# Kernel tuning notes

Hardware: AMD Instinct MI355X
Metric: run time of the kernel (lower is better)

Reference implementation:

```python
import jax, jax.numpy as jnp
import numpy as np

N_NODES = 20000
N_EDGES = 320000
D_IN = 256      # n_source_nodes (input feature dim)
HEADS = 4
HEAD_DIM = 64   # n_target_nodes // heads
D_OUT = HEADS * HEAD_DIM  # n_target_nodes = 256
EDGE_DIM = 1


def setup_inputs() -> dict:
    key = jax.random.key(0)
    ks = jax.random.split(key, 12)
    s = 0.05
    return {
        "x": jax.random.normal(ks[0], (N_NODES, D_IN), jnp.float32),
        "edge_index": jax.random.randint(ks[1], (2, N_EDGES), 0, N_NODES, jnp.int64),
        "edge_attr": jax.random.normal(ks[2], (N_EDGES, EDGE_DIM), jnp.float32),
        # TransformerConv params (weights stored [in, out]; PyG Linear defaults: q/k/v have bias, edge lin has no bias, skip lin has bias)
        "Wq": jax.random.normal(ks[3], (D_IN, D_OUT), jnp.float32) * s,
        "bq": jnp.zeros((D_OUT,), jnp.float32),
        "Wk": jax.random.normal(ks[4], (D_IN, D_OUT), jnp.float32) * s,
        "bk": jnp.zeros((D_OUT,), jnp.float32),
        "Wv": jax.random.normal(ks[5], (D_IN, D_OUT), jnp.float32) * s,
        "bv": jnp.zeros((D_OUT,), jnp.float32),
        "We": jax.random.normal(ks[6], (EDGE_DIM, D_OUT), jnp.float32) * s,
        "Wskip": jax.random.normal(ks[7], (D_IN, D_OUT), jnp.float32) * s,
        "bskip": jnp.zeros((D_OUT,), jnp.float32),
        # GraphNorm params
        "gn_weight": jnp.ones((D_OUT,), jnp.float32),
        "gn_bias": jnp.zeros((D_OUT,), jnp.float32),
        "gn_mean_scale": jnp.ones((D_OUT,), jnp.float32),
    }


def reference(x, edge_index, edge_attr, Wq, bq, Wk, bk, Wv, bv, We, Wskip, bskip, gn_weight, gn_bias, gn_mean_scale):
    N = x.shape[0]
    src, dst = edge_index[0], edge_index[1]  # message flows src -> dst (source_to_target)

    q = (x @ Wq + bq).reshape(N, HEADS, HEAD_DIM)
    k = (x @ Wk + bk).reshape(N, HEADS, HEAD_DIM)
    v = (x @ Wv + bv).reshape(N, HEADS, HEAD_DIM)
    e = (edge_attr @ We).reshape(-1, HEADS, HEAD_DIM)  # [E, H, C]

    k_j = k[src] + e                                   # [E, H, C]
    alpha = jnp.einsum('ehc,ehc->eh', q[dst], k_j) / jnp.sqrt(jnp.float32(HEAD_DIM))

    # segment softmax over edges sharing the same target node
    a_max = jax.ops.segment_max(alpha, dst, num_segments=N)[dst]
    a_exp = jnp.exp(alpha - a_max)
    a_sum = jax.ops.segment_sum(a_exp, dst, num_segments=N)[dst]
    att = a_exp / (a_sum + 1e-16)                      # [E, H]

    msg = (v[src] + e) * att[..., None]                # [E, H, C]
    out = jax.ops.segment_sum(msg, dst, num_segments=N).reshape(N, D_OUT)
    out = out + x @ Wskip + bskip                      # root/skip connection (beta=False)

    # GraphNorm (single graph): weight*(x - alpha*mean)/sqrt(var+eps) + bias
    mean = out.mean(axis=0)
    centered = out - gn_mean_scale * mean
    var = jnp.mean(centered * centered, axis=0)
    out = gn_weight * centered * jax.lax.rsqrt(var + 1e-5) + gn_bias

    out = jax.nn.relu(out)
    xt = out.T @ out                                   # [D_OUT, D_OUT]
    xt_min, xt_max = jnp.min(xt), jnp.max(xt)
    return (xt - xt_min) / (xt_max - xt_min + 1e-8)
```

## Files before the change

kernel.cpp:

```cpp
#include <hip/hip_runtime.h>
#include <math.h>

#define N_NODES 20000
#define N_EDGES 320000
#define SK 20480
#define APAD 80
#define GPITCH 144
#define KVROW 768

typedef short short8 __attribute__((ext_vector_type(8)));
typedef float f32x4 __attribute__((ext_vector_type(4)));
typedef float f32x2 __attribute__((ext_vector_type(2)));

static __device__ __forceinline__ unsigned short f2bf(float f) {
    unsigned int u = __float_as_uint(f);
    u = (u + 0x7FFF + ((u >> 16) & 1)) >> 16;
    return (unsigned short)u;
}
static __device__ __forceinline__ float b2f(unsigned short u) {
    return __uint_as_float((unsigned int)u << 16);
}

__global__ __launch_bounds__(256) void prep_k(const float* __restrict__ x,
                                              unsigned short* __restrict__ xb,
                                              const float* __restrict__ Wq,
                                              const float* __restrict__ Wk,
                                              const float* __restrict__ Wv,
                                              const float* __restrict__ Wsk,
                                              const float* __restrict__ bq,
                                              const float* __restrict__ bk,
                                              const float* __restrict__ bv,
                                              const float* __restrict__ bsk,
                                              unsigned short* __restrict__ wT,
                                              float* __restrict__ bias_all,
                                              int* __restrict__ deg)
{
    const int b = blockIdx.x;
    const int tid = threadIdx.x;
    if (b < 2500) {
        const size_t base = ((size_t)b * 256 + tid) * 8;
        const float4 f0 = *(const float4*)(x + base);
        const float4 f1 = *(const float4*)(x + base + 4);
        ushort4 u0, u1;
        u0.x = f2bf(f0.x); u0.y = f2bf(f0.y); u0.z = f2bf(f0.z); u0.w = f2bf(f0.w);
        u1.x = f2bf(f1.x); u1.y = f2bf(f1.y); u1.z = f2bf(f1.z); u1.w = f2bf(f1.w);
        *(ushort4*)(xb + base) = u0;
        *(ushort4*)(xb + base + 4) = u1;
    } else if (b < 3524) {
        const int bb = b - 2500;
        const int wi = bb >> 8, n = bb & 255;
        const float* W = (wi == 0) ? Wq : (wi == 1) ? Wk : (wi == 2) ? Wv : Wsk;
        wT[(size_t)bb * 256 + tid] = f2bf(W[(size_t)tid * 256 + n]);
        if (tid == 0) {
            const float* bv_ = (wi == 0) ? bq : (wi == 1) ? bk : (wi == 2) ? bv : bsk;
            bias_all[bb] = bv_[n];
        }
    } else {
        const int i = (b - 3524) * 256 + tid;
        if (i < N_NODES) deg[i] = 0;
    }
}

__global__ void count_deg(const int* __restrict__ dst, int* __restrict__ deg)
{
    const int e = blockIdx.x * 256 + threadIdx.x;
    if (e < N_EDGES) atomicAdd(&deg[dst[e]], 1);
}

__global__ __launch_bounds__(256, 4) void gemm_qkvs(const unsigned short* __restrict__ xb,
                                                    const unsigned short* __restrict__ wT,
                                                    const float* __restrict__ bias_all,
                                                    unsigned short* __restrict__ qb,
                                                    unsigned char* __restrict__ kvb,
                                                    unsigned short* __restrict__ ob)
{
    __shared__ __align__(16) unsigned short As[(128 + 128) * APAD];
    unsigned short* Bs = As + 128 * APAD;
    float* stage = (float*)As;

    const int tid  = threadIdx.x;
    const int lane = tid & 63;
    const int w    = tid >> 6;
    const int wm = w >> 1, wn = w & 1;
    const int row0 = blockIdx.x * 128;
    const int by   = blockIdx.y;
    const int wsel = by >> 1;
    const int ar = tid >> 1, ak = (tid & 1) * 32;
    const int fr = lane & 15, fk = (lane >> 4) * 8, lg = lane >> 4;

    int gr = row0 + ar; gr = gr < N_NODES ? gr : N_NODES - 1;
    const unsigned short* ab = xb + (size_t)gr * 256 + ak;
    const unsigned short* bb = wT + (size_t)(by * 128 + ar) * 256 + ak;

    f32x4 acc[4][4] = {};
    uint4 a0, a1, a2, a3, b0, b1, b2, b3;

    a0 = *(const uint4*)ab;        a1 = *(const uint4*)(ab + 8);
    a2 = *(const uint4*)(ab + 16); a3 = *(const uint4*)(ab + 24);
    b0 = *(const uint4*)bb;        b1 = *(const uint4*)(bb + 8);
    b2 = *(const uint4*)(bb + 16); b3 = *(const uint4*)(bb + 24);

#pragma unroll
    for (int it = 0; it < 4; ++it) {
        __syncthreads();
        unsigned short* asp = &As[ar * APAD + ak];
        *(uint4*)asp        = a0;
        *(uint4*)(asp + 8)  = a1;
        *(uint4*)(asp + 16) = a2;
        *(uint4*)(asp + 24) = a3;
        unsigned short* bsp = &Bs[ar * APAD + ak];
        *(uint4*)bsp        = b0;
        *(uint4*)(bsp + 8)  = b1;
        *(uint4*)(bsp + 16) = b2;
        *(uint4*)(bsp + 24) = b3;
        __syncthreads();
        if (it < 3) {
            const unsigned short* ap = ab + (it + 1) * 64;
            const unsigned short* bp = bb + (it + 1) * 64;
            a0 = *(const uint4*)ap;        a1 = *(const uint4*)(ap + 8);
            a2 = *(const uint4*)(ap + 16); a3 = *(const uint4*)(ap + 24);
            b0 = *(const uint4*)bp;        b1 = *(const uint4*)(bp + 8);
            b2 = *(const uint4*)(bp + 16); b3 = *(const uint4*)(bp + 24);
        }
#pragma unroll
        for (int ks = 0; ks < 2; ++ks) {
            short8 af[4], bf[4];
#pragma unroll
            for (int m = 0; m < 4; ++m)
                af[m] = *(const short8*)&As[(wm * 64 + m * 16 + fr) * APAD + ks * 32 + fk];
#pragma unroll
            for (int n = 0; n < 4; ++n)
                bf[n] = *(const short8*)&Bs[(wn * 64 + n * 16 + fr) * APAD + ks * 32 + fk];
#pragma unroll
            for (int m = 0; m < 4; ++m)
#pragma unroll
                for (int n = 0; n < 4; ++n)
                    acc[m][n] = __builtin_amdgcn_mfma_f32_16x16x32_bf16(af[m], bf[n], acc[m][n], 0, 0, 0);
        }
    }
    __syncthreads();

    float badd[4];
#pragma unroll
    for (int n = 0; n < 4; ++n) badd[n] = bias_all[by * 128 + wn * 64 + n * 16 + fr];

    float* st = stage + w * 1024;
    const int chalf = by & 1;
#pragma unroll
    for (int m = 0; m < 4; ++m) {
#pragma unroll
        for (int n = 0; n < 4; ++n)
#pragma unroll
            for (int r = 0; r < 4; ++r)
                st[(lg * 4 + r) * 64 + n * 16 + fr] = acc[m][n][r] + badd[n];
#pragma unroll
        for (int it = 0; it < 4; ++it) {
            const int lrow = it * 4 + lg;
            const f32x4 c4 = *(const f32x4*)&st[lrow * 64 + fr * 4];
            const int grow = row0 + wm * 64 + m * 16 + lrow;
            if (grow < N_NODES) {
                const int colin = chalf * 128 + wn * 64 + fr * 4;
                if (wsel == 1) {
                    int pk = __builtin_amdgcn_cvt_pk_fp8_f32(c4[0], c4[1], 0, false);
                    pk = __builtin_amdgcn_cvt_pk_fp8_f32(c4[2], c4[3], pk, true);
                    *(unsigned int*)(kvb + (size_t)grow * KVROW + colin) = (unsigned int)pk;
                } else {
                    ushort4 u;
                    u.x = f2bf(c4[0]); u.y = f2bf(c4[1]); u.z = f2bf(c4[2]); u.w = f2bf(c4[3]);
                    if (wsel == 3) {
                        *(ushort4*)(ob + (size_t)grow * 256 + colin) = u;
                    } else if (wsel == 0) {
                        *(ushort4*)(qb + (size_t)grow * 256 + colin) = u;
                    } else {
                        *(ushort4*)(kvb + (size_t)grow * KVROW + 256 + colin * 2) = u;
                    }
                }
            }
        }
    }
}

__global__ __launch_bounds__(1024) void scan_k(const int* __restrict__ deg,
                                               int* __restrict__ row_start,
                                               int* __restrict__ cursor)
{
    __shared__ int sdeg[20480];
    const int tid = threadIdx.x;
    const int lane = tid & 63, wid = tid >> 6;
    const int CH = 20;
#pragma unroll
    for (int i = 0; i < 20; ++i) {
        const int idx = i * 1024 + tid;
        sdeg[idx] = (idx < N_NODES) ? deg[idx] : 0;
    }
    __syncthreads();
    const int base = tid * CH;
    int local[CH];
    int s = 0;
#pragma unroll
    for (int i = 0; i < CH; ++i) {
        local[i] = s;
        s += sdeg[base + i];
    }
    int v = s;
#pragma unroll
    for (int off = 1; off < 64; off <<= 1) {
        const int t = __shfl_up(v, off);
        if (lane >= off) v += t;
    }
    __shared__ int wsum[16];
    if (lane == 63) wsum[wid] = v;
    __syncthreads();
    if (tid == 0) {
        int r = 0;
        for (int i = 0; i < 16; ++i) { const int t = wsum[i]; wsum[i] = r; r += t; }
    }
    __syncthreads();
    const int excl = v - s + wsum[wid];
#pragma unroll
    for (int i = 0; i < CH; ++i) {
        const int idx = base + i;
        if (idx < N_NODES) {
            row_start[idx] = excl + local[i];
            cursor[idx] = 0;
        }
    }
    if (tid == 1023) row_start[N_NODES] = excl + s;
}

__global__ void fill_csr(const int* __restrict__ dst, const int* __restrict__ src,
                         const float* __restrict__ ea,
                         const int* __restrict__ row_start,
                         int* __restrict__ cursor, int2* __restrict__ ekv,
                         float* __restrict__ gstats)
{
    const int g = blockIdx.x * 256 + threadIdx.x;
    if (g < 512) gstats[g] = 0.f;
    const int e = g;
    if (e < N_EDGES) {
        const int d = dst[e];
        const int p = atomicAdd(&cursor[d], 1);
        int2 pk;
        pk.x = src[e];
        pk.y = __float_as_int(ea[e]);
        ekv[row_start[d] + p] = pk;
    }
}

static __device__ __forceinline__ void edge_step(const unsigned int ku, const ushort4 vv,
                                                 const float a,
                                                 const float4 qf, const float4 we4,
                                                 float& ssum, float& ax, float& ay,
                                                 float& az, float& aw)
{
    const f32x2 k01 = __builtin_amdgcn_cvt_pk_f32_fp8((int)ku, false);
    const f32x2 k23 = __builtin_amdgcn_cvt_pk_f32_fp8((int)ku, true);
    float p = qf.x * (k01[0] + a * we4.x) + qf.y * (k01[1] + a * we4.y)
            + qf.z * (k23[0] + a * we4.z) + qf.w * (k23[1] + a * we4.w);
    p += __shfl_xor(p, 1); p += __shfl_xor(p, 2);
    p += __shfl_xor(p, 4); p += __shfl_xor(p, 8);
    const float wgt = __expf(p * 0.125f);
    ssum += wgt;
    ax += wgt * (b2f(vv.x) + a * we4.x);
    ay += wgt * (b2f(vv.y) + a * we4.y);
    az += wgt * (b2f(vv.z) + a * we4.z);
    aw += wgt * (b2f(vv.w) + a * we4.w);
}

__global__ __launch_bounds__(256) void attn_k(const unsigned short* __restrict__ qb,
                                              const unsigned char* __restrict__ kvb,
                                              const float* __restrict__ We,
                                              const int* __restrict__ row_start,
                                              const int2* __restrict__ ekv,
                                              unsigned short* __restrict__ out)
{
    const int wid  = threadIdx.x >> 6;
    const int lane = threadIdx.x & 63;
    const int n = blockIdx.x * 4 + wid;

    const ushort4 qv = *(const ushort4*)(qb + (size_t)n * 256 + lane * 4);
    float4 qf;
    qf.x = b2f(qv.x); qf.y = b2f(qv.y); qf.z = b2f(qv.z); qf.w = b2f(qv.w);
    const float4 we4 = *(const float4*)(We + lane * 4);
    const int rs = row_start[n], re = row_start[n + 1];
    const int koff = lane << 2;
    const int voff = 256 + (lane << 3);

    float ssum = 0.f;
    float ax = 0.f, ay = 0.f, az = 0.f, aw = 0.f;

    int s = rs;
    for (; s + 4 <= re; s += 4) {
        const int2 p0 = ekv[s],     p1 = ekv[s + 1];
        const int2 p2 = ekv[s + 2], p3 = ekv[s + 3];
        const unsigned char* r0p = kvb + (size_t)p0.x * KVROW;
        const unsigned char* r1p = kvb + (size_t)p1.x * KVROW;
        const unsigned char* r2p = kvb + (size_t)p2.x * KVROW;
        const unsigned char* r3p = kvb + (size_t)p3.x * KVROW;
        const unsigned int k0 = *(const unsigned int*)(r0p + koff);
        const ushort4      v0 = *(const ushort4*)(r0p + voff);
        const unsigned int k1 = *(const unsigned int*)(r1p + koff);
        const ushort4      v1 = *(const ushort4*)(r1p + voff);
        const unsigned int k2 = *(const unsigned int*)(r2p + koff);
        const ushort4      v2 = *(const ushort4*)(r2p + voff);
        const unsigned int k3 = *(const unsigned int*)(r3p + koff);
        const ushort4      v3 = *(const ushort4*)(r3p + voff);
        edge_step(k0, v0, __int_as_float(p0.y), qf, we4, ssum, ax, ay, az, aw);
        edge_step(k1, v1, __int_as_float(p1.y), qf, we4, ssum, ax, ay, az, aw);
        edge_step(k2, v2, __int_as_float(p2.y), qf, we4, ssum, ax, ay, az, aw);
        edge_step(k3, v3, __int_as_float(p3.y), qf, we4, ssum, ax, ay, az, aw);
    }
    for (; s < re; ++s) {
        const int2 p0 = ekv[s];
        const unsigned char* r0p = kvb + (size_t)p0.x * KVROW;
        const unsigned int k0 = *(const unsigned int*)(r0p + koff);
        const ushort4      v0 = *(const ushort4*)(r0p + voff);
        edge_step(k0, v0, __int_as_float(p0.y), qf, we4, ssum, ax, ay, az, aw);
    }
    const float inv = 1.f / (ssum + 1e-16f);
    const ushort4 sk4 = *(const ushort4*)(out + (size_t)n * 256 + lane * 4);
    ushort4 ou;
    ou.x = f2bf(ax * inv + b2f(sk4.x));
    ou.y = f2bf(ay * inv + b2f(sk4.y));
    ou.z = f2bf(az * inv + b2f(sk4.z));
    ou.w = f2bf(aw * inv + b2f(sk4.w));
    *(ushort4*)(out + (size_t)n * 256 + lane * 4) = ou;
}

__global__ __launch_bounds__(256) void gn_stats_k(const unsigned short* __restrict__ out,
                                                  float* __restrict__ gstats)
{
    const int c = threadIdx.x;
    float s = 0.f, s2 = 0.f;
    for (int r = blockIdx.x; r < N_NODES; r += gridDim.x) {
        const float vv = b2f(out[(size_t)r * 256 + c]);
        s += vv; s2 += vv * vv;
    }
    atomicAdd(&gstats[c], s);
    atomicAdd(&gstats[256 + c], s2);
}

__global__ __launch_bounds__(256) void norm_relu_T(const unsigned short* __restrict__ ob,
                                                   const float* __restrict__ gstats,
                                                   const float* __restrict__ gw,
                                                   const float* __restrict__ gb,
                                                   const float* __restrict__ gms,
                                                   unsigned short* __restrict__ obT,
                                                   float* __restrict__ xt)
{
    __shared__ unsigned short tile[256][72];
    __shared__ float smu[256], swi[256], sbd[256];
    const int t = threadIdx.x;
    const int r0 = blockIdx.x * 64;
    {
        const int zi = blockIdx.x * 256 + t;
        if (zi < 65536) xt[zi] = 0.f;
    }
    {
        const float invN = 1.f / (float)N_NODES;
        const float mean = gstats[t] * invN;
        const float exx  = gstats[256 + t] * invN;
        const float mu   = gms[t] * mean;
        const float var  = exx - 2.f * mu * mean + mu * mu;
        smu[t] = mu;
        swi[t] = gw[t] * rsqrtf(var + 1e-5f);
        sbd[t] = gb[t];
    }
    __syncthreads();
    const int rr = t >> 2;
    const int row = r0 + rr;
#pragma unroll
    for (int it = 0; it < 16; ++it) {
        const int col = it * 16 + (t & 3) * 4;
        ushort4 u;
        if (row < N_NODES) {
            const ushort4 uv = *(const ushort4*)(ob + (size_t)row * 256 + col);
            u.x = f2bf(fmaxf((b2f(uv.x) - smu[col + 0]) * swi[col + 0] + sbd[col + 0], 0.f));
            u.y = f2bf(fmaxf((b2f(uv.y) - smu[col + 1]) * swi[col + 1] + sbd[col + 1], 0.f));
            u.z = f2bf(fmaxf((b2f(uv.z) - smu[col + 2]) * swi[col + 2] + sbd[col + 2], 0.f));
            u.w = f2bf(fmaxf((b2f(uv.w) - smu[col + 3]) * swi[col + 3] + sbd[col + 3], 0.f));
        } else { u.x = u.y = u.z = u.w = 0; }
        tile[col + 0][rr] = u.x;
        tile[col + 1][rr] = u.y;
        tile[col + 2][rr] = u.z;
        tile[col + 3][rr] = u.w;
    }
    __syncthreads();
#pragma unroll
    for (int it = 0; it < 8; ++it) {
        const int c = it * 32 + (t >> 3);
        const int part = t & 7;
        const uint4 x0 = *(const uint4*)&tile[c][part * 8];
        *(uint4*)(obT + (size_t)c * SK + r0 + part * 8) = x0;
    }
}

__global__ __launch_bounds__(256) void gram_k(const unsigned short* __restrict__ obT,
                                              float* __restrict__ xt)
{
    const int bi_l[10] = {0,0,0,0,1,1,1,2,2,3};
    const int bj_l[10] = {0,1,2,3,1,2,3,2,3,3};
    const int bi = bi_l[blockIdx.x], bj = bj_l[blockIdx.x];
    const int r0 = blockIdx.y * 256;

    __shared__ __align__(16) unsigned short Ai[64 * GPITCH];
    __shared__ __align__(16) unsigned short Aj[64 * GPITCH];
    const int tid = threadIdx.x;
    const int lane = tid & 63;
    const int w = tid >> 6;
    const int wi = w >> 1, wj = w & 1;
    const int lr = tid >> 2, kseg = (tid & 3) * 32;
    const int fr = lane & 15, fk = (lane >> 4) * 8, lg = lane >> 4;

    f32x4 acc[2][2] = {};

    const unsigned short* pa = obT + (size_t)(bi * 64 + lr) * SK + r0 + kseg;
    const unsigned short* pb = obT + (size_t)(bj * 64 + lr) * SK + r0 + kseg;
    uint4 ai[4], aj[4];
#pragma unroll
    for (int j = 0; j < 4; ++j) { ai[j] = *(const uint4*)(pa + 8 * j); aj[j] = *(const uint4*)(pb + 8 * j); }

#pragma unroll
    for (int itr = 0; itr < 2; ++itr) {
        __syncthreads();
#pragma unroll
        for (int j = 0; j < 4; ++j) {
            *(uint4*)&Ai[lr * GPITCH + kseg + 8 * j] = ai[j];
            *(uint4*)&Aj[lr * GPITCH + kseg + 8 * j] = aj[j];
        }
        __syncthreads();
        if (itr == 0) {
#pragma unroll
            for (int j = 0; j < 4; ++j) {
                ai[j] = *(const uint4*)(pa + 128 + 8 * j);
                aj[j] = *(const uint4*)(pb + 128 + 8 * j);
            }
        }
#pragma unroll
        for (int ks = 0; ks < 4; ++ks) {
            short8 af[2], bf[2];
#pragma unroll
            for (int m = 0; m < 2; ++m)
                af[m] = *(const short8*)&Ai[(wi * 32 + m * 16 + fr) * GPITCH + ks * 32 + fk];
#pragma unroll
            for (int n = 0; n < 2; ++n)
                bf[n] = *(const short8*)&Aj[(wj * 32 + n * 16 + fr) * GPITCH + ks * 32 + fk];
#pragma unroll
            for (int m = 0; m < 2; ++m)
#pragma unroll
                for (int n = 0; n < 2; ++n)
                    acc[m][n] = __builtin_amdgcn_mfma_f32_16x16x32_bf16(af[m], bf[n], acc[m][n], 0, 0, 0);
        }
    }
#pragma unroll
    for (int m = 0; m < 2; ++m)
#pragma unroll
        for (int n = 0; n < 2; ++n)
#pragma unroll
            for (int r = 0; r < 4; ++r)
                atomicAdd(&xt[(size_t)(bi * 64 + wi * 32 + m * 16 + lg * 4 + r) * 256
                              + bj * 64 + wj * 32 + n * 16 + fr], acc[m][n][r]);
}

__global__ __launch_bounds__(1024) void minmax_fin_k(const float* __restrict__ xt,
                                                     float* __restrict__ outp)
{
    const int tid = threadIdx.x;
    float mn = 1e30f, mx = -1e30f;
    for (int i = tid; i < 65536; i += 1024) {
        const int r = i >> 8, c = i & 255;
        if ((r >> 6) <= (c >> 6)) {
            const float v = xt[i];
            mn = fminf(mn, v);
            mx = fmaxf(mx, v);
        }
    }
    for (int off = 1; off < 64; off <<= 1) {
        mn = fminf(mn, __shfl_xor(mn, off));
        mx = fmaxf(mx, __shfl_xor(mx, off));
    }
    __shared__ float smn[16], smx[16];
    __shared__ float fmn, fmx;
    const int w = tid >> 6;
    if ((tid & 63) == 0) { smn[w] = mn; smx[w] = mx; }
    __syncthreads();
    if (tid == 0) {
        for (int i = 1; i < 16; ++i) {
            mn = fminf(mn, smn[i]);
            mx = fmaxf(mx, smx[i]);
        }
        fmn = mn; fmx = mx;
    }
    __syncthreads();
    const float gmn = fmn;
    const float inv = 1.f / (fmx - gmn + 1e-8f);
    for (int i = tid; i < 65536; i += 1024) {
        const int r = i >> 8, c = i & 255;
        const float v = ((r >> 6) <= (c >> 6)) ? xt[i] : xt[c * 256 + r];
        outp[i] = (v - gmn) * inv;
    }
}

extern "C" void kernel_launch(void* const* d_in, const int* in_sizes, int n_in,
                              void* d_out, int out_size, void* d_ws, size_t ws_size,
                              hipStream_t stream)
{
    (void)in_sizes; (void)n_in; (void)out_size; (void)ws_size;
    const float* x   = (const float*)d_in[0];
    const int*   ei  = (const int*)d_in[1];
    const float* ea  = (const float*)d_in[2];
    const float* Wq  = (const float*)d_in[3];
    const float* bq  = (const float*)d_in[4];
    const float* Wk  = (const float*)d_in[5];
    const float* bk  = (const float*)d_in[6];
    const float* Wv  = (const float*)d_in[7];
    const float* bv  = (const float*)d_in[8];
    const float* We  = (const float*)d_in[9];
    const float* Wsk = (const float*)d_in[10];
    const float* bsk = (const float*)d_in[11];
    const float* gw  = (const float*)d_in[12];
    const float* gb  = (const float*)d_in[13];
    const float* gms = (const float*)d_in[14];
    float* outp = (float*)d_out;

    char* ws = (char*)d_ws;
    size_t off = 0;
    #define WS_ALLOC(nbytes) (ws + off); off = (off + (size_t)(nbytes) + 255) & ~(size_t)255
    unsigned short* xb  = (unsigned short*)WS_ALLOC((size_t)N_NODES * 256 * 2);
    unsigned short* wT  = (unsigned short*)WS_ALLOC((size_t)1024 * 256 * 2);
    float* bias_all     = (float*)WS_ALLOC(1024 * 4);
    unsigned short* qb  = (unsigned short*)WS_ALLOC((size_t)N_NODES * 256 * 2);
    unsigned char*  kvb = (unsigned char*)WS_ALLOC((size_t)N_NODES * KVROW);
    unsigned short* ob  = (unsigned short*)WS_ALLOC((size_t)N_NODES * 256 * 2);
    int*   deg          = (int*)WS_ALLOC((size_t)N_NODES * 4);
    int*   cur          = (int*)WS_ALLOC((size_t)N_NODES * 4);
    float* gstats       = (float*)WS_ALLOC(512 * 4);
    float* xt           = (float*)WS_ALLOC(65536 * 4);
    int* row_start      = (int*)WS_ALLOC((size_t)(N_NODES + 1) * 4);
    #undef WS_ALLOC
    int2* ekv           = (int2*)xb;
    unsigned short* obT = (unsigned short*)xb;

    const int* srcv = ei;
    const int* dstv = ei + N_EDGES;

    prep_k<<<2500 + 1024 + 79, 256, 0, stream>>>(x, xb, Wq, Wk, Wv, Wsk,
                                                 bq, bk, bv, bsk, wT, bias_all, deg);

    count_deg<<<(N_EDGES + 255) / 256, 256, 0, stream>>>(dstv, deg);

    gemm_qkvs<<<dim3((N_NODES + 127) / 128, 8), 256, 0, stream>>>(xb, wT, bias_all,
                                                                  qb, kvb, ob);

    scan_k<<<1, 1024, 0, stream>>>(deg, row_start, cur);
    fill_csr<<<(N_EDGES + 255) / 256, 256, 0, stream>>>(dstv, srcv, ea, row_start,
                                                        cur, ekv, gstats);

    attn_k<<<N_NODES / 4, 256, 0, stream>>>(qb, kvb, We, row_start, ekv, ob);

    gn_stats_k<<<400, 256, 0, stream>>>(ob, gstats);
    norm_relu_T<<<320, 256, 0, stream>>>(ob, gstats, gw, gb, gms, obT, xt);

    gram_k<<<dim3(10, 80), 256, 0, stream>>>(obT, xt);
    minmax_fin_k<<<1, 1024, 0, stream>>>(xt, outp);
}
```

Baseline: 224.8 us.

## Fold degree counting into QKV GEMM and load MFMA operands directly from global

Removes the separate count_deg launch by adding an extra grid row (blockIdx.y==8) to the QKV/skip GEMM that does the atomic degree histogram with a grid-stride loop. The GEMM drops its shared-memory A/B tiling and barriers: each lane now reads its MFMA fragments straight from global/L2. The epilogue staging buffer gets a padded pitch to avoid LDS bank conflicts, and launch bounds drop to 2 blocks per SM. This saves a launch and the LDS sync overhead, but issues more redundant, less coalesced global loads and may lower occupancy.

Result: slower. 231.7 us (+3.1%).

```diff
diff --git a/kernel.cpp b/kernel.cpp
--- a/kernel.cpp
+++ b/kernel.cpp
@@ -4,9 +4,9 @@
 #define N_NODES 20000
 #define N_EDGES 320000
 #define SK 20480
-#define APAD 80
 #define GPITCH 144
 #define KVROW 768
+#define SP 68
 
 typedef short short8 __attribute__((ext_vector_type(8)));
 typedef float f32x4 __attribute__((ext_vector_type(4)));
@@ -61,102 +61,76 @@
     }
 }
 
-__global__ void count_deg(const int* __restrict__ dst, int* __restrict__ deg)
-{
-    const int e = blockIdx.x * 256 + threadIdx.x;
-    if (e < N_EDGES) atomicAdd(&deg[dst[e]], 1);
-}
-
-__global__ __launch_bounds__(256, 4) void gemm_qkvs(const unsigned short* __restrict__ xb,
+__global__ __launch_bounds__(256, 2) void gemm_qkvs(const unsigned short* __restrict__ xb,
                                                     const unsigned short* __restrict__ wT,
                                                     const float* __restrict__ bias_all,
                                                     unsigned short* __restrict__ qb,
                                                     unsigned char* __restrict__ kvb,
-                                                    unsigned short* __restrict__ ob)
-{
-    __shared__ __align__(16) unsigned short As[(128 + 128) * APAD];
-    unsigned short* Bs = As + 128 * APAD;
-    float* stage = (float*)As;
-
+                                                    unsigned short* __restrict__ ob,
+                                                    const int* __restrict__ dst,
+                                                    int* __restrict__ deg)
+{
     const int tid  = threadIdx.x;
+    const int by   = blockIdx.y;
+    if (by == 8) {
+        for (int e = blockIdx.x * 256 + tid; e < N_EDGES; e += 157 * 256)
+            atomicAdd(&deg[dst[e]], 1);
+        return;
+    }
+
+    __shared__ float stage[4 * 16 * SP];
+
     const int lane = tid & 63;
     const int w    = tid >> 6;
     const int wm = w >> 1, wn = w & 1;
     const int row0 = blockIdx.x * 128;
-    const int by   = blockIdx.y;
     const int wsel = by >> 1;
-    const int ar = tid >> 1, ak = (tid & 1) * 32;
+    const int chalf = by & 1;
     const int fr = lane & 15, fk = (lane >> 4) * 8, lg = lane >> 4;
 
-    int gr = row0 + ar; gr = gr < N_NODES ? gr : N_NODES - 1;
-    const unsigned short* ab = xb + (size_t)gr * 256 + ak;
-    const unsigned short* bb = wT + (size_t)(by * 128 + ar) * 256 + ak;
+    const unsigned short* ap[4];
+    const unsigned short* bp[4];
+#pragma unroll
+    for (int m = 0; m < 4; ++m) {
+        int r = row0 + wm * 64 + m * 16 + fr;
+        r = r < N_NODES ? r : N_NODES - 1;
+        ap[m] = xb + (size_t)r * 256 + fk;
+    }
+#pragma unroll
+    for (int n = 0; n < 4; ++n)
+        bp[n] = wT + (size_t)(by * 128 + wn * 64 + n * 16 + fr) * 256 + fk;
 
     f32x4 acc[4][4] = {};
-    uint4 a0, a1, a2, a3, b0, b1, b2, b3;
-
-    a0 = *(const uint4*)ab;        a1 = *(const uint4*)(ab + 8);
-    a2 = *(const uint4*)(ab + 16); a3 = *(const uint4*)(ab + 24);
-    b0 = *(const uint4*)bb;        b1 = *(const uint4*)(bb + 8);
-    b2 = *(const uint4*)(bb + 16); b3 = *(const uint4*)(bb + 24);
-
-#pragma unroll
-    for (int it = 0; it < 4; ++it) {
-        __syncthreads();
-        unsigned short* asp = &As[ar * APAD + ak];
-        *(uint4*)asp        = a0;
-        *(uint4*)(asp + 8)  = a1;
-        *(uint4*)(asp + 16) = a2;
-        *(uint4*)(asp + 24) = a3;
-        unsigned short* bsp = &Bs[ar * APAD + ak];
-        *(uint4*)bsp        = b0;
-        *(uint4*)(bsp + 8)  = b1;
-        *(uint4*)(bsp + 16) = b2;
-        *(uint4*)(bsp + 24) = b3;
-        __syncthreads();
-        if (it < 3) {
-            const unsigned short* ap = ab + (it + 1) * 64;
-            const unsigned short* bp = bb + (it + 1) * 64;
-            a0 = *(const uint4*)ap;        a1 = *(const uint4*)(ap + 8);
-            a2 = *(const uint4*)(ap + 16); a3 = *(const uint4*)(ap + 24);
-            b0 = *(const uint4*)bp;        b1 = *(const uint4*)(bp + 8);
-            b2 = *(const uint4*)(bp + 16); b3 = *(const uint4*)(bp + 24);
-        }
-#pragma unroll
-        for (int ks = 0; ks < 2; ++ks) {
-            short8 af[4], bf[4];
-#pragma unroll
-            for (int m = 0; m < 4; ++m)
-                af[m] = *(const short8*)&As[(wm * 64 + m * 16 + fr) * APAD + ks * 32 + fk];
+#pragma unroll
+    for (int ks = 0; ks < 8; ++ks) {
+        short8 af[4], bf[4];
+#pragma unroll
+        for (int m = 0; m < 4; ++m) af[m] = *(const short8*)(ap[m] + ks * 32);
+#pragma unroll
+        for (int n = 0; n < 4; ++n) bf[n] = *(const short8*)(bp[n] + ks * 32);
+#pragma unroll
+        for (int m = 0; m < 4; ++m)
 #pragma unroll
             for (int n = 0; n < 4; ++n)
-                bf[n] = *(const short8*)&Bs[(wn * 64 + n * 16 + fr) * APAD + ks * 32 + fk];
-#pragma unroll
-            for (int m = 0; m < 4; ++m)
-#pragma unroll
-                for (int n = 0; n < 4; ++n)
-                    acc[m][n] = __builtin_amdgcn_mfma_f32_16x16x32_bf16(af[m], bf[n], acc[m][n], 0, 0, 0);
-        }
-    }
-    __syncthreads();
+                acc[m][n] = __builtin_amdgcn_mfma_f32_16x16x32_bf16(af[m], bf[n], acc[m][n], 0, 0, 0);
+    }
 
     float badd[4];
 #pragma unroll
     for (int n = 0; n < 4; ++n) badd[n] = bias_all[by * 128 + wn * 64 + n * 16 + fr];
 
-    float* st = stage + w * 1024;
-    const int chalf = by & 1;
+    float* st = stage + w * (16 * SP);
 #pragma unroll
     for (int m = 0; m < 4; ++m) {
 #pragma unroll
         for (int n = 0; n < 4; ++n)
 #pragma unroll
             for (int r = 0; r < 4; ++r)
-                st[(lg * 4 + r) * 64 + n * 16 + fr] = acc[m][n][r] + badd[n];
+                st[(lg * 4 + r) * SP + n * 16 + fr] = acc[m][n][r] + badd[n];
 #pragma unroll
         for (int it = 0; it < 4; ++it) {
             const int lrow = it * 4 + lg;
-            const f32x4 c4 = *(const f32x4*)&st[lrow * 64 + fr * 4];
+            const f32x4 c4 = *(const f32x4*)&st[lrow * SP + fr * 4];
             const int grow = row0 + wm * 64 + m * 16 + lrow;
             if (grow < N_NODES) {
                 const int colin = chalf * 128 + wn * 64 + fr * 4;
@@ -547,10 +521,8 @@
     prep_k<<<2500 + 1024 + 79, 256, 0, stream>>>(x, xb, Wq, Wk, Wv, Wsk,
                                                  bq, bk, bv, bsk, wT, bias_all, deg);
 
-    count_deg<<<(N_EDGES + 255) / 256, 256, 0, stream>>>(dstv, deg);
-
-    gemm_qkvs<<<dim3((N_NODES + 127) / 128, 8), 256, 0, stream>>>(xb, wT, bias_all,
-                                                                  qb, kvb, ob);
+    gemm_qkvs<<<dim3(157, 9), 256, 0, stream>>>(xb, wT, bias_all,
+                                                qb, kvb, ob, dstv, deg);
 
     scan_k<<<1, 1024, 0, stream>>>(deg, row_start, cur);
     fill_csr<<<(N_EDGES + 255) / 256, 256, 0, stream>>>(dstv, srcv, ea, row_start,
```

## Tile weight transpose through shared memory and fold degree counting into GEMM launch

Applied to the files above, without the earlier changes.

The weight transpose in the prep kernel now uses 64x64 shared-memory tiles, giving coalesced reads and writes in place of strided per-column reads across 1024 blocks. The separate degree-count kernel is removed. Its atomics now run in an extra row of blocks (blockIdx.y==8) of the QKV/skip GEMM launch, which saves one kernel launch and lets the atomics overlap with GEMM work. The cost is a shared array declared in the prep kernel that every block allocates, plus atomic traffic contending with the GEMM blocks.

Result: faster. 217.0 us (-3.5%).

```diff
diff --git a/kernel.cpp b/kernel.cpp
--- a/kernel.cpp
+++ b/kernel.cpp
@@ -35,6 +35,7 @@
                                               float* __restrict__ bias_all,
                                               int* __restrict__ deg)
 {
+    __shared__ float tw[64][65];
     const int b = blockIdx.x;
     const int tid = threadIdx.x;
     if (b < 2500) {
@@ -46,25 +47,33 @@
         u1.x = f2bf(f1.x); u1.y = f2bf(f1.y); u1.z = f2bf(f1.z); u1.w = f2bf(f1.w);
         *(ushort4*)(xb + base) = u0;
         *(ushort4*)(xb + base + 4) = u1;
-    } else if (b < 3524) {
-        const int bb = b - 2500;
-        const int wi = bb >> 8, n = bb & 255;
+    } else if (b < 2564) {
+        const int b2 = b - 2500;
+        const int wi = b2 >> 4;
+        const int t2 = b2 & 15;
+        const int n0 = (t2 & 3) * 64;
+        const int k0 = (t2 >> 2) * 64;
         const float* W = (wi == 0) ? Wq : (wi == 1) ? Wk : (wi == 2) ? Wv : Wsk;
-        wT[(size_t)bb * 256 + tid] = f2bf(W[(size_t)tid * 256 + n]);
-        if (tid == 0) {
+        const int r = tid >> 6, c = tid & 63;
+#pragma unroll
+        for (int it = 0; it < 16; ++it) {
+            const int row = it * 4 + r;
+            tw[row][c] = W[(size_t)(k0 + row) * 256 + n0 + c];
+        }
+        __syncthreads();
+#pragma unroll
+        for (int it = 0; it < 16; ++it) {
+            const int n = it * 4 + r;
+            wT[(size_t)(wi * 256 + n0 + n) * 256 + k0 + c] = f2bf(tw[c][n]);
+        }
+        if (k0 == 0 && tid < 64) {
             const float* bv_ = (wi == 0) ? bq : (wi == 1) ? bk : (wi == 2) ? bv : bsk;
-            bias_all[bb] = bv_[n];
+            bias_all[wi * 256 + n0 + tid] = bv_[n0 + tid];
         }
     } else {
-        const int i = (b - 3524) * 256 + tid;
+        const int i = (b - 2564) * 256 + tid;
         if (i < N_NODES) deg[i] = 0;
     }
-}
-
-__global__ void count_deg(const int* __restrict__ dst, int* __restrict__ deg)
-{
-    const int e = blockIdx.x * 256 + threadIdx.x;
-    if (e < N_EDGES) atomicAdd(&deg[dst[e]], 1);
 }
 
 __global__ __launch_bounds__(256, 4) void gemm_qkvs(const unsigned short* __restrict__ xb,
@@ -72,18 +81,26 @@
                                                     const float* __restrict__ bias_all,
                                                     unsigned short* __restrict__ qb,
                                                     unsigned char* __restrict__ kvb,
-                                                    unsigned short* __restrict__ ob)
-{
+                                                    unsigned short* __restrict__ ob,
+                                                    const int* __restrict__ dst,
+                                                    int* __restrict__ deg)
+{
+    const int tid  = threadIdx.x;
+    const int by   = blockIdx.y;
+    if (by == 8) {
+        for (int e = blockIdx.x * 256 + tid; e < N_EDGES; e += 157 * 256)
+            atomicAdd(&deg[dst[e]], 1);
+        return;
+    }
+
     __shared__ __align__(16) unsigned short As[(128 + 128) * APAD];
     unsigned short* Bs = As + 128 * APAD;
     float* stage = (float*)As;
 
-    const int tid  = threadIdx.x;
     const int lane = tid & 63;
     const int w    = tid >> 6;
     const int wm = w >> 1, wn = w & 1;
     const int row0 = blockIdx.x * 128;
-    const int by   = blockIdx.y;
     const int wsel = by >> 1;
     const int ar = tid >> 1, ak = (tid & 1) * 32;
     const int fr = lane & 15, fk = (lane >> 4) * 8, lg = lane >> 4;
@@ -544,13 +561,11 @@
     const int* srcv = ei;
     const int* dstv = ei + N_EDGES;
 
-    prep_k<<<2500 + 1024 + 79, 256, 0, stream>>>(x, xb, Wq, Wk, Wv, Wsk,
-                                                 bq, bk, bv, bsk, wT, bias_all, deg);
-
-    count_deg<<<(N_EDGES + 255) / 256, 256, 0, stream>>>(dstv, deg);
-
-    gemm_qkvs<<<dim3((N_NODES + 127) / 128, 8), 256, 0, stream>>>(xb, wT, bias_all,
-                                                                  qb, kvb, ob);
+    prep_k<<<2500 + 64 + 79, 256, 0, stream>>>(x, xb, Wq, Wk, Wv, Wsk,
+                                               bq, bk, bv, bsk, wT, bias_all, deg);
+
+    gemm_qkvs<<<dim3(157, 9), 256, 0, stream>>>(xb, wT, bias_all,
+                                                qb, kvb, ob, dstv, deg);
 
     scan_k<<<1, 1024, 0, stream>>>(deg, row_start, cur);
     fill_csr<<<(N_EDGES + 255) / 256, 256, 0, stream>>>(dstv, srcv, ea, row_start,
```
